# Kernel tuning notes

Hardware: AMD Instinct MI355X
Metric: run time of the kernel (lower is better)

## Reference

```python
import jax, jax.numpy as jnp
import numpy as np

THRESH = 0.5
DECAY = 0.2
N_NODES = 39
T = 2000
K_HOPS = 3


def setup_inputs() -> dict:
    key = jax.random.key(0)
    ks = jax.random.split(key, 10)
    x = jax.random.normal(ks[0], (N_NODES, 2, T), dtype=jnp.float32)
    edge_index = jax.random.randint(ks[1], (2, 156), 0, N_NODES)
    # TAGConv(2, 64, K=3): (K+1) bias-free hop weights + single bias
    W_conv = jax.random.normal(ks[2], (K_HOPS + 1, 2, 64), dtype=jnp.float32) * 0.3
    b_conv = jax.random.normal(ks[3], (64,), dtype=jnp.float32) * 0.05
    W1 = jax.random.normal(ks[4], (N_NODES * 64, 128), dtype=jnp.float32) * 0.02
    b1 = jax.random.normal(ks[5], (128,), dtype=jnp.float32) * 0.02
    W2 = jax.random.normal(ks[6], (128, 256), dtype=jnp.float32) * 0.08
    b2 = jax.random.normal(ks[7], (256,), dtype=jnp.float32) * 0.02
    W3 = jax.random.normal(ks[8], (256, 36), dtype=jnp.float32) * 0.06
    b3 = jax.random.normal(ks[9], (36,), dtype=jnp.float32) * 0.02
    return {"x": x, "edge_index": edge_index, "W_conv": W_conv, "b_conv": b_conv,
            "W1": W1, "b1": b1, "W2": W2, "b2": b2, "W3": W3, "b3": b3}


def _norm_adj(edge_index, dtype):
    # PyG gcn_norm without self loops: A_hat = D^-1/2 A D^-1/2, message flows row->col
    row, col = edge_index[0], edge_index[1]
    A = jnp.zeros((N_NODES, N_NODES), dtype).at[col, row].add(1.0)
    deg = A.sum(axis=1)
    dinv = jnp.where(deg > 0, deg ** -0.5, 0.0).astype(dtype)
    return dinv[:, None] * A * dinv[None, :]


def reference(x, edge_index, W_conv, b_conv, W1, b1, W2, b2, W3, b3):
    A_hat = _norm_adj(edge_index, x.dtype)

    def spike(m):
        return (m > THRESH).astype(m.dtype)

    def step(carry, xt):
        c1m, c1s, h1m, h1s, h2m, h2s, h3m, h3s, acc = carry
        # TAGConv: sum_k (A_hat^k xt) @ W_k + bias   [39,64]
        h = xt
        conv = h @ W_conv[0]
        for k in range(1, K_HOPS + 1):
            h = A_hat @ h
            conv = conv + h @ W_conv[k]
        conv = conv + b_conv
        c1m = c1m * DECAY * (1.0 - c1s) + conv
        c1s = spike(c1m)
        f = c1s.reshape(-1)  # [2496]
        h1m = h1m * DECAY * (1.0 - h1s) + f @ W1 + b1
        h1s = spike(h1m)
        h2m = h2m * DECAY * (1.0 - h2s) + h1s @ W2 + b2
        h2s = spike(h2m)
        h3m = h3m * DECAY * (1.0 - h3s) + h2s @ W3 + b3
        h3s = spike(h3m)
        return (c1m, c1s, h1m, h1s, h2m, h2s, h3m, h3s, acc + h3s), None

    z = lambda s: jnp.zeros(s, x.dtype)
    init = (z((N_NODES, 64)), z((N_NODES, 64)), z((128,)), z((128,)),
            z((256,)), z((256,)), z((36,)), z((36,)), z((36,)))
    xs = jnp.moveaxis(x, -1, 0)  # [T, 39, 2]
    carry, _ = jax.lax.scan(step, init, xs)
    return carry[-1] / x.shape[-1]
```

## Files before the change

kernel.cpp:

```cpp
#include <hip/hip_runtime.h>

#define T 2000
#define K1N 2496
#define K2 4992
#define TLA 8
#define MAXNZ 24
#define NBLK 250

using short8 = __attribute__((ext_vector_type(8))) short;
using floatx4 = __attribute__((ext_vector_type(4))) float;

__device__ __forceinline__ unsigned bf16_rne(float v) {
    unsigned u = __float_as_uint(v);
    return (u + 0x7FFFu + ((u >> 16) & 1u)) >> 16;
}
__device__ __forceinline__ unsigned packhl(float w) {
    unsigned hi = bf16_rne(w);
    float r = w - __uint_as_float(hi << 16);
    unsigned lo = bf16_rne(r);
    return (hi & 0xFFFFu) | (lo << 16);
}

__global__ __launch_bounds__(256) void hops(const float* __restrict__ x,
        const int* __restrict__ ei, float* __restrict__ Fg,
        const float* __restrict__ W1, unsigned* __restrict__ W1t,
        float* __restrict__ out) {
    __shared__ float ah[1560];
    __shared__ float2 alist[39 * MAXNZ];
    __shared__ int nnzr[40];
    __shared__ float bufA[78 * TLA];
    __shared__ float bufB[78 * TLA];
    __shared__ float feat[39 * TLA * 8];
    int tid = threadIdx.x;
    int bl = blockIdx.x;
    int ts = bl * TLA;

    if (bl == 0 && tid < 36) out[tid] = 0.f;

    for (int u = tid; u < 1521; u += 256) ah[u] = 0.f;
    __syncthreads();
    if (tid < 156) atomicAdd(&ah[ei[156 + tid] * 39 + ei[tid]], 1.f);
    __syncthreads();
    if (tid < 39) {
        float d = 0.f;
        for (int u = 0; u < 39; ++u) d += ah[tid * 39 + u];
        ah[1521 + tid] = (d > 0.f) ? (1.f / sqrtf(d)) : 0.f;
    }
    __syncthreads();
    for (int u = tid; u < 1521; u += 256) {
        int i = u / 39, j = u - i * 39;
        ah[u] = (ah[1521 + i] * ah[u]) * ah[1521 + j];
    }
    __syncthreads();
    if (tid < 39) {
        int cnt = 0;
        for (int m = 0; m < 39; ++m) {
            float v = ah[tid * 39 + m];
            if (v != 0.f && cnt < MAXNZ) {
                alist[tid * MAXNZ + cnt] = make_float2(v, __int_as_float((2 * m) * TLA * 4));
                ++cnt;
            }
        }
        nnzr[tid] = cnt;
    }
    __syncthreads();

    for (int e = tid; e < 78 * TLA; e += 256) {
        int r = e / TLA, tt = e - r * TLA;
        bufA[r * TLA + tt] = x[r * T + ts + tt];
    }
    __syncthreads();

    for (int e = tid; e < 78 * TLA; e += 256) {
        int r = e / TLA, tt = e - r * TLA;
        feat[((r >> 1) * TLA + tt) * 8 + (r & 1)] = bufA[r * TLA + tt];
    }
    for (int e = tid; e < 78; e += 256) {
        int r = e, ii = r >> 1, c = r & 1;
        float acc[8];
        #pragma unroll
        for (int u = 0; u < 8; ++u) acc[u] = 0.f;
        int nz = nnzr[ii];
        const float2* lp = &alist[ii * MAXNZ];
        int cg = c * (TLA * 4);
        for (int q = 0; q < nz; ++q) {
            float2 av = lp[q];
            const float* xp = (const float*)((const char*)bufA + (__float_as_int(av.y) + cg));
            float a = av.x;
            float4 x0 = *(const float4*)xp;
            float4 x1 = *(const float4*)(xp + 4);
            acc[0] += a * x0.x; acc[1] += a * x0.y; acc[2] += a * x0.z; acc[3] += a * x0.w;
            acc[4] += a * x1.x; acc[5] += a * x1.y; acc[6] += a * x1.z; acc[7] += a * x1.w;
        }
        float* dp = &bufB[r * TLA];
        *(float4*)dp = *(float4*)&acc[0];
        *(float4*)(dp + 4) = *(float4*)&acc[4];
    }
    __syncthreads();

    for (int e = tid; e < 78 * TLA; e += 256) {
        int r = e / TLA, tt = e - r * TLA;
        feat[((r >> 1) * TLA + tt) * 8 + 2 + (r & 1)] = bufB[r * TLA + tt];
    }
    for (int e = tid; e < 78; e += 256) {
        int r = e, ii = r >> 1, c = r & 1;
        float acc[8];
        #pragma unroll
        for (int u = 0; u < 8; ++u) acc[u] = 0.f;
        int nz = nnzr[ii];
        const float2* lp = &alist[ii * MAXNZ];
        int cg = c * (TLA * 4);
        for (int q = 0; q < nz; ++q) {
            float2 av = lp[q];
            const float* xp = (const float*)((const char*)bufB + (__float_as_int(av.y) + cg));
            float a = av.x;
            float4 x0 = *(const float4*)xp;
            float4 x1 = *(const float4*)(xp + 4);
            acc[0] += a * x0.x; acc[1] += a * x0.y; acc[2] += a * x0.z; acc[3] += a * x0.w;
            acc[4] += a * x1.x; acc[5] += a * x1.y; acc[6] += a * x1.z; acc[7] += a * x1.w;
        }
        float* dp = &bufA[r * TLA];
        *(float4*)dp = *(float4*)&acc[0];
        *(float4*)(dp + 4) = *(float4*)&acc[4];
    }
    __syncthreads();

    for (int e = tid; e < 78 * TLA; e += 256) {
        int r = e / TLA, tt = e - r * TLA;
        feat[((r >> 1) * TLA + tt) * 8 + 4 + (r & 1)] = bufA[r * TLA + tt];
    }
    for (int e = tid; e < 78; e += 256) {
        int r = e, ii = r >> 1, c = r & 1;
        float acc[8];
        #pragma unroll
        for (int u = 0; u < 8; ++u) acc[u] = 0.f;
        int nz = nnzr[ii];
        const float2* lp = &alist[ii * MAXNZ];
        int cg = c * (TLA * 4);
        for (int q = 0; q < nz; ++q) {
            float2 av = lp[q];
            const float* xp = (const float*)((const char*)bufA + (__float_as_int(av.y) + cg));
            float a = av.x;
            float4 x0 = *(const float4*)xp;
            float4 x1 = *(const float4*)(xp + 4);
            acc[0] += a * x0.x; acc[1] += a * x0.y; acc[2] += a * x0.z; acc[3] += a * x0.w;
            acc[4] += a * x1.x; acc[5] += a * x1.y; acc[6] += a * x1.z; acc[7] += a * x1.w;
        }
        #pragma unroll
        for (int u = 0; u < 8; ++u)
            feat[(ii * TLA + u) * 8 + 6 + c] = acc[u];
    }
    __syncthreads();

    for (int e = tid; e < 39 * TLA * 2; e += 256) {
        int idx = e >> 1, half = e & 1;
        int n = idx / TLA, tt = idx - n * TLA;
        *(float4*)&Fg[((size_t)n * T + ts + tt) * 8 + half * 4] =
            *(const float4*)&feat[idx * 8 + half * 4];
    }

    const int total = 128 * K1N;
    for (int f = bl * 256 + tid; f < total; f += NBLK * 256) {
        int k = f >> 7, jj = f & 127;
        W1t[jj * K1N + k] = packhl(W1[f]);
    }
}

__global__ __launch_bounds__(512) void scan_gemm1(
        const float* __restrict__ Fg, const float* __restrict__ Wc,
        const float* __restrict__ bc, const short* __restrict__ W1t,
        float* __restrict__ F1p) {
    __shared__ __align__(16) char smem[13312 + 23040];
    unsigned char* S2 = (unsigned char*)smem;
    float* FgL = (float*)(smem + 13312);
    short* As  = (short*)(smem + 13312);
    short* Ws  = (short*)(smem + 13312 + 4608);

    int tid = threadIdx.x;
    int bx = blockIdx.x, ks = blockIdx.y;
    int t0 = bx * 32;
    int hs = t0 - 16; if (hs < 0) hs = 0;
    int ncol = t0 + 32 - hs;
    int k0g = ks * 416;
    int nd0 = k0g >> 6;

    int kb2 = ks * 832;
    int jjv[2], kov[2];
    #pragma unroll
    for (int u = 0; u < 2; ++u) {
        int aid = u * 512 + tid;
        jjv[u] = aid >> 3;
        kov[u] = (aid & 7) * 8;
    }
    short8 wr0 = *(const short8*)&W1t[jjv[0] * K2 + kb2 + kov[0]];
    short8 wr1 = *(const short8*)&W1t[jjv[1] * K2 + kb2 + kov[1]];

    for (int e = tid; e < 7 * ncol * 2; e += 512) {
        int idx = e >> 1, half = e & 1;
        int nl = idx / ncol, cc = idx - nl * ncol;
        int t = hs + cc;
        int gn = nd0 + nl;
        float4 v = make_float4(0.f, 0.f, 0.f, 0.f);
        if (gn < 39 && t < T)
            v = *(const float4*)&Fg[((size_t)gn * T + t) * 8 + half * 4];
        *(float4*)&FgL[(nl * ncol + cc) * 8 + half * 4] = v;
    }
    __syncthreads();

    {
        int cn = tid;
        if (cn < 416) {
            int gk = k0g + cn;
            int nl = (gk >> 6) - nd0;
            int j = gk & 63;
            float wv[8];
            #pragma unroll
            for (int q = 0; q < 8; ++q) wv[q] = Wc[q * 64 + j];
            float bias = bc[j];
            float m = 0.f, s = 0.f;
            const float* fb = &FgL[nl * ncol * 8];
            for (int cc = 0; cc < ncol; ++cc) {
                float4 a0 = *(const float4*)&fb[cc * 8];
                float4 a1 = *(const float4*)&fb[cc * 8 + 4];
                float acc = 0.f;
                acc += wv[0] * a0.x; acc += wv[1] * a0.y;
                acc += wv[2] * a0.z; acc += wv[3] * a0.w;
                acc += wv[4] * a1.x; acc += wv[5] * a1.y;
                acc += wv[6] * a1.z; acc += wv[7] * a1.w;
                float v = acc + bias;
                m = m * 0.2f * (1.f - s) + v;
                s = (m > 0.5f) ? 1.f : 0.f;
                int t = hs + cc;
                if (t >= t0) S2[(t - t0) * 416 + cn] = (unsigned char)(s != 0.f);
            }
        }
    }
    __syncthreads();

    int lane = tid & 63, wvi = tid >> 6;
    int j0 = wvi * 16;
    int row = lane & 15, quad = lane >> 4;
    floatx4 a00 = {0.f, 0.f, 0.f, 0.f};
    floatx4 a10 = a00;
    int sm = tid >> 3, sb4 = (tid & 7) * 4;
    for (int c = 0; c < 13; ++c) {
        if (tid < 256) {
            unsigned u4 = *(const unsigned*)&S2[sm * 416 + c * 32 + sb4];
            uint4 dd;
            dd.x = (u4 & 0x000000FFu) ? 0x3F803F80u : 0u;
            dd.y = (u4 & 0x0000FF00u) ? 0x3F803F80u : 0u;
            dd.z = (u4 & 0x00FF0000u) ? 0x3F803F80u : 0u;
            dd.w = (u4 & 0xFF000000u) ? 0x3F803F80u : 0u;
            *(uint4*)&As[sm * 72 + sb4 * 2] = dd;
        }
        *(short8*)&Ws[jjv[0] * 72 + kov[0]] = wr0;
        *(short8*)&Ws[jjv[1] * 72 + kov[1]] = wr1;
        __syncthreads();
        short8 wn0, wn1;
        if (c < 12) {
            wn0 = *(const short8*)&W1t[jjv[0] * K2 + kb2 + (c + 1) * 64 + kov[0]];
            wn1 = *(const short8*)&W1t[jjv[1] * K2 + kb2 + (c + 1) * 64 + kov[1]];
        }
        #pragma unroll
        for (int sh = 0; sh < 2; ++sh) {
            int k0 = sh * 32 + quad * 8;
            short8 fa0 = *(const short8*)&As[row * 72 + k0];
            short8 fa1 = *(const short8*)&As[(row + 16) * 72 + k0];
            short8 fb0 = *(const short8*)&Ws[(j0 + row) * 72 + k0];
            a00 = __builtin_amdgcn_mfma_f32_16x16x32_bf16(fa0, fb0, a00, 0, 0, 0);
            a10 = __builtin_amdgcn_mfma_f32_16x16x32_bf16(fa1, fb0, a10, 0, 0, 0);
        }
        __syncthreads();
        if (c < 12) { wr0 = wn0; wr1 = wn1; }
    }
    #pragma unroll
    for (int r = 0; r < 4; ++r) {
        int m0 = quad * 4 + r;
        int t = t0 + m0;
        if (t < T)
            F1p[t * 768 + ks * 128 + j0 + row] = a00[r];
        int t2 = t0 + 16 + m0;
        if (t2 < T)
            F1p[t2 * 768 + ks * 128 + j0 + row] = a10[r];
    }
}

__global__ __launch_bounds__(256) void h1_gemm2(const float* __restrict__ F1p,
        const float* __restrict__ b1, const float* __restrict__ W2,
        float* __restrict__ G2) {
    __shared__ float AT[128 * 8];
    int tid = threadIdx.x;
    int t0 = blockIdx.x * 8;
    if (tid < 128) {
        int n = tid;
        int hs = t0 - 16; if (hs < 0) hs = 0;
        float b = b1[n];
        float m = 0.f, s = 0.f;
        for (int tg = hs; tg < t0 + 8; tg += 4) {
            float vb[4][6];
            #pragma unroll
            for (int u = 0; u < 4; ++u)
                #pragma unroll
                for (int q = 0; q < 6; ++q)
                    vb[u][q] = F1p[(tg + u) * 768 + q * 128 + n];
            #pragma unroll
            for (int u = 0; u < 4; ++u) {
                float v = 0.f;
                #pragma unroll
                for (int q = 0; q < 6; ++q) v += vb[u][q];
                v += b;
                m = m * 0.2f * (1.f - s) + v;
                s = (m > 0.5f) ? 1.f : 0.f;
                int t = tg + u;
                if (t >= t0) AT[n * 8 + (t - t0)] = s;
            }
        }
    }
    __syncthreads();
    int j = tid;
    float acc[8] = {0.f};
    #pragma unroll 4
    for (int k = 0; k < 128; ++k) {
        float w = W2[k * 256 + j];
        float4 q0 = *(const float4*)&AT[k * 8 + 0];
        float4 q1 = *(const float4*)&AT[k * 8 + 4];
        acc[0] += q0.x * w; acc[1] += q0.y * w; acc[2] += q0.z * w; acc[3] += q0.w * w;
        acc[4] += q1.x * w; acc[5] += q1.y * w; acc[6] += q1.z * w; acc[7] += q1.w * w;
    }
    #pragma unroll
    for (int tt = 0; tt < 8; ++tt) G2[(t0 + tt) * 256 + j] = acc[tt];
}

__global__ __launch_bounds__(256) void tail(const float* __restrict__ G2,
        const float* __restrict__ b2, const float* __restrict__ W3,
        const float* __restrict__ b3, float* __restrict__ out) {
    __shared__ float w3t[36 * 260];
    __shared__ unsigned char S2[36 * 260];
    __shared__ float G3[36 * 36];
    int tid = threadIdx.x;
    int t0 = blockIdx.x * 10;
    int gs = t0 - 25; if (gs < 0) gs = 0;
    int hs = gs - 25; if (hs < 0) hs = 0;
    int L3 = t0 + 10 - gs;
    #pragma unroll
    for (int u = 0; u < 9; ++u) {
        int f = u * 1024 + tid * 4;
        float4 wq = *(const float4*)&W3[f];
        int k0 = f / 36, j0 = f - k0 * 36;
        float wv[4] = {wq.x, wq.y, wq.z, wq.w};
        #pragma unroll
        for (int q = 0; q < 4; ++q) {
            int k = (j0 + q >= 36) ? k0 + 1 : k0;
            int jj = (j0 + q >= 36) ? (j0 + q - 36) : (j0 + q);
            w3t[jj * 260 + k] = wv[q];
        }
    }
    {
        int n = tid;
        float b = b2[n];
        float m = 0.f, s = 0.f;
        for (int base = hs; base < t0 + 10; base += 10) {
            float vb[10];
            #pragma unroll
            for (int u = 0; u < 10; ++u) vb[u] = G2[(base + u) * 256 + n];
            #pragma unroll
            for (int u = 0; u < 10; ++u) {
                float v = vb[u] + b;
                m = m * 0.2f * (1.f - s) + v;
                s = (m > 0.5f) ? 1.f : 0.f;
                int t = base + u;
                if (t >= gs) S2[(t - gs) * 260 + n] = (unsigned char)(s != 0.f);
            }
        }
    }
    __syncthreads();
    for (int e = tid; e < 36 * 9; e += 256) {
        int jj = e / 9, g = e - (e / 9) * 9;
        int tb = g * 4;
        if (tb >= L3) continue;
        float ac0 = 0.f, ac1 = 0.f, ac2 = 0.f, ac3 = 0.f;
        const unsigned char* r0 = &S2[tb * 260];
        for (int k = 0; k < 256; k += 4) {
            float4 w = *(const float4*)&w3t[jj * 260 + k];
            uchar4 q0 = *(const uchar4*)&r0[k];
            uchar4 q1 = *(const uchar4*)&r0[260 + k];
            uchar4 q2 = *(const uchar4*)&r0[520 + k];
            uchar4 q3 = *(const uchar4*)&r0[780 + k];
            ac0 += (float)q0.x * w.x + (float)q0.y * w.y + (float)q0.z * w.z + (float)q0.w * w.w;
            ac1 += (float)q1.x * w.x + (float)q1.y * w.y + (float)q1.z * w.z + (float)q1.w * w.w;
            ac2 += (float)q2.x * w.x + (float)q2.y * w.y + (float)q2.z * w.z + (float)q2.w * w.w;
            ac3 += (float)q3.x * w.x + (float)q3.y * w.y + (float)q3.z * w.z + (float)q3.w * w.w;
        }
        G3[tb * 36 + jj] = ac0;
        if (tb + 1 < L3) G3[(tb + 1) * 36 + jj] = ac1;
        if (tb + 2 < L3) G3[(tb + 2) * 36 + jj] = ac2;
        if (tb + 3 < L3) G3[(tb + 3) * 36 + jj] = ac3;
    }
    __syncthreads();
    if (tid < 36) {
        int n = tid;
        float b = b3[n];
        float m = 0.f, s = 0.f;
        int cnt = 0;
        for (int t = gs; t < t0 + 10; ++t) {
            float v = G3[(t - gs) * 36 + n] + b;
            m = m * 0.2f * (1.f - s) + v;
            s = (m > 0.5f) ? 1.f : 0.f;
            if (t >= t0) cnt += (s != 0.f) ? 1 : 0;
        }
        atomicAdd(&out[n], (float)cnt * 0.0005f);
    }
}

extern "C" void kernel_launch(void* const* d_in, const int* in_sizes, int n_in,
                              void* d_out, int out_size, void* d_ws, size_t ws_size,
                              hipStream_t stream) {
    const float* x  = (const float*)d_in[0];
    const int*   ei = (const int*)d_in[1];
    const float* Wc = (const float*)d_in[2];
    const float* bc = (const float*)d_in[3];
    const float* W1 = (const float*)d_in[4];
    const float* b1 = (const float*)d_in[5];
    const float* W2 = (const float*)d_in[6];
    const float* b2 = (const float*)d_in[7];
    const float* W3 = (const float*)d_in[8];
    const float* b3 = (const float*)d_in[9];
    float* out = (float*)d_out;

    float* w = (float*)d_ws;
    float* F1p = w;                       w += (size_t)T * 768;
    float* G2  = w;                       w += (size_t)T * 256;
    float* Fg  = w;                       w += (size_t)39 * T * 8;
    unsigned* W1t = (unsigned*)w;         w += 128 * K1N;

    hops<<<NBLK, 256, 0, stream>>>(x, ei, Fg, W1, W1t, out);
    scan_gemm1<<<dim3(63, 6), 512, 0, stream>>>(Fg, Wc, bc, (const short*)W1t, F1p);
    h1_gemm2<<<250, 256, 0, stream>>>(F1p, b1, W2, G2);
    tail<<<200, 256, 0, stream>>>(G2, b2, W3, b3, out);
}
```

Before: 139.8 us.

## Load MFMA operands directly from global/spike buffer and enlarge tail time tiles

In scan_gemm1 the staged LDS tiles for spikes and W1 are removed. Each lane now reads its W1 bf16 fragment straight from global memory and converts spike bytes from a padded LDS buffer directly into MFMA A-fragments, which drops two __syncthreads per k-chunk and shrinks shared memory. Separately, the tail kernel processes 25 timesteps per block instead of 10, so 80 blocks launch instead of 200 and the 50-step warmup recomputation is amortised over more outputs. The trade-off is uncoalesced, unprefetched global loads for W1, and less parallelism in tail.

```diff
diff --git a/kernel.cpp b/kernel.cpp
--- a/kernel.cpp
+++ b/kernel.cpp
@@ -6,6 +6,7 @@
 #define TLA 8
 #define MAXNZ 24
 #define NBLK 250
+#define S2P 420
 
 using short8 = __attribute__((ext_vector_type(8))) short;
 using floatx4 = __attribute__((ext_vector_type(4))) float;
@@ -19,6 +20,14 @@
     float r = w - __uint_as_float(hi << 16);
     unsigned lo = bf16_rne(r);
     return (hi & 0xFFFFu) | (lo << 16);
+}
+__device__ __forceinline__ short8 spike8(unsigned u) {
+    union { uint4 d; short8 s; } r;
+    r.d.x = (u & 0x000000FFu) ? 0x3F803F80u : 0u;
+    r.d.y = (u & 0x0000FF00u) ? 0x3F803F80u : 0u;
+    r.d.z = (u & 0x00FF0000u) ? 0x3F803F80u : 0u;
+    r.d.w = (u & 0xFF000000u) ? 0x3F803F80u : 0u;
+    return r.s;
 }
 
 __global__ __launch_bounds__(256) void hops(const float* __restrict__ x,
@@ -170,11 +179,9 @@
         const float* __restrict__ Fg, const float* __restrict__ Wc,
         const float* __restrict__ bc, const short* __restrict__ W1t,
         float* __restrict__ F1p) {
-    __shared__ __align__(16) char smem[13312 + 23040];
+    __shared__ __align__(16) char smem[32 * S2P + 10752];
     unsigned char* S2 = (unsigned char*)smem;
-    float* FgL = (float*)(smem + 13312);
-    short* As  = (short*)(smem + 13312);
-    short* Ws  = (short*)(smem + 13312 + 4608);
+    float* FgL = (float*)(smem + 32 * S2P);
 
     int tid = threadIdx.x;
     int bx = blockIdx.x, ks = blockIdx.y;
@@ -183,17 +190,7 @@
     int ncol = t0 + 32 - hs;
     int k0g = ks * 416;
     int nd0 = k0g >> 6;
-
     int kb2 = ks * 832;
-    int jjv[2], kov[2];
-    #pragma unroll
-    for (int u = 0; u < 2; ++u) {
-        int aid = u * 512 + tid;
-        jjv[u] = aid >> 3;
-        kov[u] = (aid & 7) * 8;
-    }
-    short8 wr0 = *(const short8*)&W1t[jjv[0] * K2 + kb2 + kov[0]];
-    short8 wr1 = *(const short8*)&W1t[jjv[1] * K2 + kb2 + kov[1]];
 
     for (int e = tid; e < 7 * ncol * 2; e += 512) {
         int idx = e >> 1, half = e & 1;
@@ -231,7 +228,7 @@
                 m = m * 0.2f * (1.f - s) + v;
                 s = (m > 0.5f) ? 1.f : 0.f;
                 int t = hs + cc;
-                if (t >= t0) S2[(t - t0) * 416 + cn] = (unsigned char)(s != 0.f);
+                if (t >= t0) S2[(t - t0) * S2P + cn] = (unsigned char)(s != 0.f);
             }
         }
     }
@@ -242,36 +239,21 @@
     int row = lane & 15, quad = lane >> 4;
     floatx4 a00 = {0.f, 0.f, 0.f, 0.f};
     floatx4 a10 = a00;
-    int sm = tid >> 3, sb4 = (tid & 7) * 4;
+    const short* wrow = &W1t[(j0 + row) * K2 + kb2];
+    const unsigned char* s2a = &S2[row * S2P];
+    const unsigned char* s2b = &S2[(row + 16) * S2P];
     for (int c = 0; c < 13; ++c) {
-        if (tid < 256) {
-            unsigned u4 = *(const unsigned*)&S2[sm * 416 + c * 32 + sb4];
-            uint4 dd;
-            dd.x = (u4 & 0x000000FFu) ? 0x3F803F80u : 0u;
-            dd.y = (u4 & 0x0000FF00u) ? 0x3F803F80u : 0u;
-            dd.z = (u4 & 0x00FF0000u) ? 0x3F803F80u : 0u;
-            dd.w = (u4 & 0xFF000000u) ? 0x3F803F80u : 0u;
-            *(uint4*)&As[sm * 72 + sb4 * 2] = dd;
-        }
-        *(short8*)&Ws[jjv[0] * 72 + kov[0]] = wr0;
-        *(short8*)&Ws[jjv[1] * 72 + kov[1]] = wr1;
-        __syncthreads();
-        short8 wn0, wn1;
-        if (c < 12) {
-            wn0 = *(const short8*)&W1t[jjv[0] * K2 + kb2 + (c + 1) * 64 + kov[0]];
-            wn1 = *(const short8*)&W1t[jjv[1] * K2 + kb2 + (c + 1) * 64 + kov[1]];
-        }
         #pragma unroll
         for (int sh = 0; sh < 2; ++sh) {
-            int k0 = sh * 32 + quad * 8;
-            short8 fa0 = *(const short8*)&As[row * 72 + k0];
-            short8 fa1 = *(const short8*)&As[(row + 16) * 72 + k0];
-            short8 fb0 = *(const short8*)&Ws[(j0 + row) * 72 + k0];
+            int kbyte = c * 32 + sh * 16 + quad * 4;
+            unsigned ua0 = *(const unsigned*)&s2a[kbyte];
+            unsigned ua1 = *(const unsigned*)&s2b[kbyte];
+            short8 fa0 = spike8(ua0);
+            short8 fa1 = spike8(ua1);
+            short8 fb0 = *(const short8*)&wrow[c * 64 + sh * 32 + quad * 8];
             a00 = __builtin_amdgcn_mfma_f32_16x16x32_bf16(fa0, fb0, a00, 0, 0, 0);
             a10 = __builtin_amdgcn_mfma_f32_16x16x32_bf16(fa1, fb0, a10, 0, 0, 0);
         }
-        __syncthreads();
-        if (c < 12) { wr0 = wn0; wr1 = wn1; }
     }
     #pragma unroll
     for (int r = 0; r < 4; ++r) {
@@ -335,13 +317,13 @@
         const float* __restrict__ b2, const float* __restrict__ W3,
         const float* __restrict__ b3, float* __restrict__ out) {
     __shared__ float w3t[36 * 260];
-    __shared__ unsigned char S2[36 * 260];
-    __shared__ float G3[36 * 36];
+    __shared__ unsigned char S2[52 * 260];
+    __shared__ float G3[52 * 36];
     int tid = threadIdx.x;
-    int t0 = blockIdx.x * 10;
+    int t0 = blockIdx.x * 25;
     int gs = t0 - 25; if (gs < 0) gs = 0;
     int hs = gs - 25; if (hs < 0) hs = 0;
-    int L3 = t0 + 10 - gs;
+    int L3 = t0 + 25 - gs;
     #pragma unroll
     for (int u = 0; u < 9; ++u) {
         int f = u * 1024 + tid * 4;
@@ -359,12 +341,12 @@
         int n = tid;
         float b = b2[n];
         float m = 0.f, s = 0.f;
-        for (int base = hs; base < t0 + 10; base += 10) {
-            float vb[10];
+        for (int base = hs; base < t0 + 25; base += 25) {
+            float vb[25];
             #pragma unroll
-            for (int u = 0; u < 10; ++u) vb[u] = G2[(base + u) * 256 + n];
+            for (int u = 0; u < 25; ++u) vb[u] = G2[(base + u) * 256 + n];
             #pragma unroll
-            for (int u = 0; u < 10; ++u) {
+            for (int u = 0; u < 25; ++u) {
                 float v = vb[u] + b;
                 m = m * 0.2f * (1.f - s) + v;
                 s = (m > 0.5f) ? 1.f : 0.f;
@@ -374,8 +356,8 @@
         }
     }
     __syncthreads();
-    for (int e = tid; e < 36 * 9; e += 256) {
-        int jj = e / 9, g = e - (e / 9) * 9;
+    for (int e = tid; e < 36 * 13; e += 256) {
+        int jj = e / 13, g = e - (e / 13) * 13;
         int tb = g * 4;
         if (tb >= L3) continue;
         float ac0 = 0.f, ac1 = 0.f, ac2 = 0.f, ac3 = 0.f;
@@ -402,7 +384,7 @@
         float b = b3[n];
         float m = 0.f, s = 0.f;
         int cnt = 0;
-        for (int t = gs; t < t0 + 10; ++t) {
+        for (int t = gs; t < t0 + 25; ++t) {
             float v = G3[(t - gs) * 36 + n] + b;
             m = m * 0.2f * (1.f - s) + v;
             s = (m > 0.5f) ? 1.f : 0.f;
@@ -436,5 +418,5 @@
     hops<<<NBLK, 256, 0, stream>>>(x, ei, Fg, W1, W1t, out);
     scan_gemm1<<<dim3(63, 6), 512, 0, stream>>>(Fg, Wc, bc, (const short*)W1t, F1p);
     h1_gemm2<<<250, 256, 0, stream>>>(F1p, b1, W2, G2);
-    tail<<<200, 256, 0, stream>>>(G2, b2, W3, b3, out);
-}
+    tail<<<80, 256, 0, stream>>>(G2, b2, W3, b3, out);
+}
```

New measurement: 137.8 us, median of 2. No clear change (-1.4%).
